# Performance work log

Hardware: AMD Instinct MI355X
Metric: run time of the kernel (lower is better)

## Reference

```python
import jax, jax.numpy as jnp
import numpy as np

B, T, D = 8, 4096, 768
H, HD, K = 12, 64, 32
TAU, THRESH = 12.5, 0.5
A_PARAM, B_PARAM, DT = 0.7, 0.8, 1.0  # nn.Parameters read via .item() -> scalar constants
N_FHN_STEPS = 2


def setup_inputs() -> dict:
    key = jax.random.key(0)
    k0, k1, k2, k3 = jax.random.split(key, 4)
    x = jax.random.normal(k0, (B, T, D), jnp.float32)
    spectral_basis = jax.random.normal(k1, (B, T, K), jnp.float32)
    w_qkv = jax.random.normal(k2, (3 * D, D), jnp.float32) * 0.02
    w_out = jax.random.normal(k3, (D, D), jnp.float32) * 0.02
    spectral_filter = jnp.ones((H, 32), jnp.float32) * 0.5
    return {"x": x, "spectral_basis": spectral_basis, "w_qkv": w_qkv,
            "w_out": w_out, "spectral_filter": spectral_filter}


def _fhn(stim):
    # Original expands stim [b,h,k] -> [b,h,k,head_dim] (constant along d), runs FHN,
    # then means over d. Values are identical along d, so amax over d == |stim| and the
    # mean is the identity; the math collapses exactly to per-element dynamics on [b,h,k].
    scale = jnp.maximum(jnp.abs(stim), 1e-6)          # == abs().amax(-1).clamp(1e-6)
    stim_normed = stim / scale
    gate = jax.nn.sigmoid((jnp.abs(stim) - THRESH) * 10.0)
    I = stim_normed * (0.1 + 0.9 * gate)
    alpha = DT / TAU
    denom = 1.0 + alpha * B_PARAM
    v = jnp.zeros_like(stim)
    w = jnp.zeros_like(stim)
    for _ in range(N_FHN_STEPS):  # fixed small n_steps, unrolled
        dv = v - (v * v * v) / 3.0 - w + I
        v_next = v + dv * DT
        w_next = (w + (v_next + A_PARAM) * alpha) / denom
        v = jnp.clip(v_next, -3.0, 3.0)
        w = jnp.clip(w_next, -3.0, 3.0)
    return v * scale


def reference(x, spectral_basis, w_qkv, w_out, spectral_filter):
    Bs, Ts, Ds = x.shape
    k = spectral_basis.shape[-1]
    qkv = x @ w_qkv.T                                   # [B,T,3D]
    qkv = qkv.reshape(Bs, Ts, 3, H, HD).transpose(2, 0, 3, 1, 4)  # three,b,h,t,d
    q, kk, v = qkv[0], qkv[1], qkv[2]
    q_spec = jnp.einsum('bhtd,btk->bhkd', q, spectral_basis)
    k_spec = jnp.einsum('bhtd,btk->bhkd', kk, spectral_basis)
    attn_spec = jnp.einsum('bhkd,bhkd->bhk', q_spec, k_spec) / (HD ** 0.5)
    filt = jax.nn.sigmoid(spectral_filter[:, :k])       # [H,k]
    attn_spec = attn_spec * filt[None, :, :]
    fhn_response = _fhn(attn_spec)                      # [B,H,k]
    v_spec = jnp.einsum('bhtd,btk->bhkd', v, spectral_basis)
    out_spec = fhn_response[..., None] * v_spec         # [B,H,k,d]
    out = jnp.einsum('bhkd,btk->bhtd', out_spec, spectral_basis)
    out = out.transpose(0, 2, 1, 3).reshape(Bs, Ts, Ds)  # b t (h d)
    return out @ w_out.T
```

## Files before the change

### kernel.cpp

```cpp
#include <hip/hip_runtime.h>

#define Bc 8
#define Tc 4096
#define Dc 768
#define Hc 12
#define HDc 64
#define Kc 32
#define TD3 2304
#define WQKV_F (TD3 * Dc)
#define WALL_F ((TD3 + Dc) * Dc)

typedef __attribute__((ext_vector_type(8))) short short8;
typedef __attribute__((ext_vector_type(4))) short short4v;
typedef __attribute__((ext_vector_type(4))) float float4v;

__device__ __forceinline__ float bf2f(unsigned short u) {
    unsigned v = ((unsigned)u) << 16;
    return __builtin_bit_cast(float, v);
}
__device__ __forceinline__ unsigned short f2bf(float f) {
    unsigned u = __builtin_bit_cast(unsigned, f);
    u += 0x7FFFu + ((u >> 16) & 1u);
    return (unsigned short)(u >> 16);
}

__device__ __forceinline__ void split8(const float* p, short8& hi, short8& lo) {
#pragma unroll
    for (int i = 0; i < 8; ++i) {
        unsigned short h = f2bf(p[i]);
        hi[i] = (short)h;
        lo[i] = (short)f2bf(p[i] - bf2f(h));
    }
}

__global__ __launch_bounds__(256) void k1_xspec(const float* __restrict__ x,
                                                const float* __restrict__ sb,
                                                float* __restrict__ pb) {
    __shared__ float xt[32 * 193];
    __shared__ float st[32 * 33];

    int tid  = threadIdx.x;
    int w    = tid >> 6;
    int lane = tid & 63;
    int col  = lane & 15;
    int quad = lane >> 4;

    int bid = blockIdx.x;
    int b  = bid >> 6;
    int dt = (bid >> 4) & 3;
    int tc = bid & 15;
    int d0 = dt * 192;
    size_t bT = (size_t)b * Tc + (size_t)tc * 256;

    float4v acc[2][3];
#pragma unroll
    for (int mi = 0; mi < 2; ++mi)
#pragma unroll
        for (int ni = 0; ni < 3; ++ni) acc[mi][ni] = (float4v){0.f, 0.f, 0.f, 0.f};

    for (int ks = 0; ks < 8; ++ks) {
        __syncthreads();
#pragma unroll
        for (int i = 0; i < 6; ++i) {
            int f4  = tid + i * 256;
            int row = f4 / 48, c4 = f4 % 48;
            float4v v = *(const float4v*)&x[(bT + ks * 32 + row) * Dc + d0 + c4 * 4];
#pragma unroll
            for (int q = 0; q < 4; ++q) xt[row * 193 + c4 * 4 + q] = v[q];
        }
        {
            int row = tid >> 3, c4 = tid & 7;
            float4v v = *(const float4v*)&sb[(bT + ks * 32 + row) * Kc + c4 * 4];
#pragma unroll
            for (int q = 0; q < 4; ++q) st[row * 33 + c4 * 4 + q] = v[q];
        }
        __syncthreads();

        short8 ah[2], al[2];
#pragma unroll
        for (int mi = 0; mi < 2; ++mi) {
            float av[8];
#pragma unroll
            for (int j = 0; j < 8; ++j)
                av[j] = st[(quad * 8 + j) * 33 + mi * 16 + col];
            split8(av, ah[mi], al[mi]);
        }
#pragma unroll
        for (int ni = 0; ni < 3; ++ni) {
            int nc = (w * 3 + ni) * 16 + col;
            float bv[8];
#pragma unroll
            for (int j = 0; j < 8; ++j)
                bv[j] = xt[(quad * 8 + j) * 193 + nc];
            short8 bh, bl;
            split8(bv, bh, bl);
#pragma unroll
            for (int mi = 0; mi < 2; ++mi) {
                acc[mi][ni] = __builtin_amdgcn_mfma_f32_16x16x32_bf16(ah[mi], bh, acc[mi][ni], 0, 0, 0);
                acc[mi][ni] = __builtin_amdgcn_mfma_f32_16x16x32_bf16(al[mi], bh, acc[mi][ni], 0, 0, 0);
                acc[mi][ni] = __builtin_amdgcn_mfma_f32_16x16x32_bf16(ah[mi], bl, acc[mi][ni], 0, 0, 0);
            }
        }
    }

    float* pbp = pb + (size_t)tc * (Bc * Kc * Dc);
#pragma unroll
    for (int mi = 0; mi < 2; ++mi)
#pragma unroll
        for (int ni = 0; ni < 3; ++ni)
#pragma unroll
            for (int r = 0; r < 4; ++r) {
                int kk = mi * 16 + quad * 4 + r;
                int dd = d0 + (w * 3 + ni) * 16 + col;
                pbp[((size_t)(b * Kc + kk)) * Dc + dd] = acc[mi][ni][r];
            }
}

__global__ __launch_bounds__(256) void k1r_reduce(const float* __restrict__ pb,
                                                  short* __restrict__ xs_hi,
                                                  short* __restrict__ xs_lo) {
    int i = (blockIdx.x * 256 + threadIdx.x) * 4;
    float4v s = (float4v){0.f, 0.f, 0.f, 0.f};
#pragma unroll
    for (int p = 0; p < 16; ++p) {
        float4v v = *(const float4v*)(pb + (size_t)p * (Bc * Kc * Dc) + i);
#pragma unroll
        for (int q = 0; q < 4; ++q) s[q] += v[q];
    }
    short4v h, l;
#pragma unroll
    for (int q = 0; q < 4; ++q) {
        unsigned short hb = f2bf(s[q]);
        h[q] = (short)hb;
        l[q] = (short)f2bf(s[q] - bf2f(hb));
    }
    *(short4v*)(xs_hi + i) = h;
    *(short4v*)(xs_lo + i) = l;
}

__global__ __launch_bounds__(256) void kconv(const float* __restrict__ wqkv,
                                             const float* __restrict__ wout,
                                             short* __restrict__ w_hi,
                                             short* __restrict__ w_lo) {
    int i = (blockIdx.x * 256 + threadIdx.x) * 4;
    const float* src = (i < WQKV_F) ? (wqkv + i) : (wout + (i - WQKV_F));
    float4v v = *(const float4v*)src;
    short4v h, l;
#pragma unroll
    for (int q = 0; q < 4; ++q) {
        unsigned short hb = f2bf(v[q]);
        h[q] = (short)hb;
        l[q] = (short)f2bf(v[q] - bf2f(hb));
    }
    *(short4v*)(w_hi + i) = h;
    *(short4v*)(w_lo + i) = l;
}

__global__ __launch_bounds__(256) void k2_qkv(const short* __restrict__ xs_hi,
                                              const short* __restrict__ xs_lo,
                                              const short* __restrict__ w_hi,
                                              const short* __restrict__ w_lo,
                                              float* __restrict__ c1) {
    int lane = threadIdx.x & 63;
    int w    = threadIdx.x >> 6;
    int m    = lane & 15, quad = lane >> 4;
    int mb = blockIdx.x & 7;
    int nb = blockIdx.x >> 3;
    int m0 = mb * 32;
    int n0 = nb * 64 + w * 16;

    const short* a0h = xs_hi + (size_t)(m0 + m) * Dc + quad * 8;
    const short* a0l = xs_lo + (size_t)(m0 + m) * Dc + quad * 8;
    const short* a1h = a0h + (size_t)16 * Dc;
    const short* a1l = a0l + (size_t)16 * Dc;
    const short* bhp = w_hi + (size_t)(n0 + m) * Dc + quad * 8;
    const short* blp = w_lo + (size_t)(n0 + m) * Dc + quad * 8;

    float4v acc0 = (float4v){0.f, 0.f, 0.f, 0.f};
    float4v acc1 = (float4v){0.f, 0.f, 0.f, 0.f};
#pragma unroll 4
    for (int s = 0; s < 24; ++s) {
        short8 bh = *(const short8*)(bhp + s * 32);
        short8 bl = *(const short8*)(blp + s * 32);
        short8 h0 = *(const short8*)(a0h + s * 32);
        short8 l0 = *(const short8*)(a0l + s * 32);
        short8 h1 = *(const short8*)(a1h + s * 32);
        short8 l1 = *(const short8*)(a1l + s * 32);
        acc0 = __builtin_amdgcn_mfma_f32_16x16x32_bf16(h0, bh, acc0, 0, 0, 0);
        acc0 = __builtin_amdgcn_mfma_f32_16x16x32_bf16(l0, bh, acc0, 0, 0, 0);
        acc0 = __builtin_amdgcn_mfma_f32_16x16x32_bf16(h0, bl, acc0, 0, 0, 0);
        acc1 = __builtin_amdgcn_mfma_f32_16x16x32_bf16(h1, bh, acc1, 0, 0, 0);
        acc1 = __builtin_amdgcn_mfma_f32_16x16x32_bf16(l1, bh, acc1, 0, 0, 0);
        acc1 = __builtin_amdgcn_mfma_f32_16x16x32_bf16(h1, bl, acc1, 0, 0, 0);
    }
    float* cp0 = c1 + (size_t)(m0 + quad * 4) * TD3 + n0 + m;
    float* cp1 = cp0 + (size_t)16 * TD3;
#pragma unroll
    for (int r = 0; r < 4; ++r) {
        cp0[(size_t)r * TD3] = acc0[r];
        cp1[(size_t)r * TD3] = acc1[r];
    }
}

__global__ __launch_bounds__(256) void k3_fhn(const float* __restrict__ c1,
                                              const float* __restrict__ sfilt,
                                              float* __restrict__ fhn) {
    int idx = blockIdx.x * 256 + threadIdx.x;
    if (idx >= Bc * Hc * Kc) return;
    int kk = idx & 31;
    int bh = idx >> 5;
    int h  = bh % Hc;
    int r  = (bh / Hc) * Kc + kk;

    const float* qp = c1 + (size_t)r * TD3 + h * HDc;
    const float* kp = qp + Dc;
    float s = 0.f;
#pragma unroll
    for (int dd = 0; dd < HDc; ++dd) s = fmaf(qp[dd], kp[dd], s);
    s *= 0.125f;

    float filt = 1.f / (1.f + __expf(-sfilt[h * 32 + kk]));
    s *= filt;

    float as    = fabsf(s);
    float scale = fmaxf(as, 1e-6f);
    float sn    = s / scale;
    float gate  = 1.f / (1.f + __expf(-(as - 0.5f) * 10.f));
    float I     = sn * (0.1f + 0.9f * gate);
    const float alpha = 0.08f;
    const float denom = 1.064f;
    float v = 0.f, w = 0.f;
#pragma unroll
    for (int it = 0; it < 2; ++it) {
        float dv = v - (v * v * v) / 3.f - w + I;
        float vn = v + dv;
        float wn = (w + (vn + 0.7f) * alpha) / denom;
        v = fminf(fmaxf(vn, -3.f), 3.f);
        w = fminf(fmaxf(wn, -3.f), 3.f);
    }
    fhn[idx] = v * scale;
}

__global__ __launch_bounds__(256) void k4_proj(const float* __restrict__ c1,
                                               const float* __restrict__ fhn,
                                               const short* __restrict__ wo_hi,
                                               const short* __restrict__ wo_lo,
                                               float* __restrict__ proj) {
    int wave = blockIdx.x * 4 + (threadIdx.x >> 6);
    int lane = threadIdx.x & 63;
    int mb = wave & 15;
    int nt = wave >> 4;
    int m0 = mb * 16, n0 = nt * 16;
    int m = lane & 15, quad = lane >> 4;

    const short* bhp = wo_hi + (size_t)(n0 + m) * Dc + quad * 8;
    const short* blp = wo_lo + (size_t)(n0 + m) * Dc + quad * 8;

    int r = m0 + m;
    int b = r >> 5, kk = r & 31;
    const float* apx = c1 + (size_t)r * TD3 + 2 * Dc + quad * 8;
    const float* fp  = fhn + (size_t)b * Hc * Kc + kk;

    float4v acc = (float4v){0.f, 0.f, 0.f, 0.f};
#pragma unroll 4
    for (int s = 0; s < 24; ++s) {
        int h = (s * 32 + quad * 8) >> 6;
        float f = fp[h * Kc];
        float av[8];
#pragma unroll
        for (int i = 0; i < 8; ++i) av[i] = apx[s * 32 + i] * f;
        short8 ah, al;
        split8(av, ah, al);
        short8 bh = *(const short8*)(bhp + s * 32);
        short8 bl = *(const short8*)(blp + s * 32);
        acc = __builtin_amdgcn_mfma_f32_16x16x32_bf16(ah, bh, acc, 0, 0, 0);
        acc = __builtin_amdgcn_mfma_f32_16x16x32_bf16(al, bh, acc, 0, 0, 0);
        acc = __builtin_amdgcn_mfma_f32_16x16x32_bf16(ah, bl, acc, 0, 0, 0);
    }
    float* cp = proj + (size_t)(m0 + quad * 4) * Dc + n0 + m;
#pragma unroll
    for (int rr = 0; rr < 4; ++rr) cp[(size_t)rr * Dc] = acc[rr];
}

__global__ __launch_bounds__(256) void k5_out(const float* __restrict__ proj,
                                              const float* __restrict__ sb,
                                              float* __restrict__ out) {
    __shared__ float pt[32 * 193];

    int tid  = threadIdx.x;
    int w    = tid >> 6;
    int lane = tid & 63;
    int col  = lane & 15;
    int quad = lane >> 4;

    int bid = blockIdx.x;
    int b  = bid >> 8;
    int tt = (bid >> 2) & 63;
    int et = bid & 3;
    int t0 = tt * 64 + w * 16;
    int e0 = et * 192;

#pragma unroll
    for (int i = 0; i < 6; ++i) {
        int f4  = tid + i * 256;
        int row = f4 / 48, c4 = f4 % 48;
        float4v v = *(const float4v*)&proj[(size_t)b * Kc * Dc + (size_t)row * Dc + e0 + c4 * 4];
#pragma unroll
        for (int q = 0; q < 4; ++q) pt[row * 193 + c4 * 4 + q] = v[q];
    }

    const float* apx = sb + ((size_t)b * Tc + t0 + col) * Kc + quad * 8;
    short8 ah, al;
    split8(apx, ah, al);

    __syncthreads();

    float4v acc[12];
#pragma unroll
    for (int ni = 0; ni < 12; ++ni) acc[ni] = (float4v){0.f, 0.f, 0.f, 0.f};

#pragma unroll
    for (int ni = 0; ni < 12; ++ni) {
        float bv[8];
#pragma unroll
        for (int j = 0; j < 8; ++j)
            bv[j] = pt[(quad * 8 + j) * 193 + ni * 16 + col];
        short8 bh, bl;
        split8(bv, bh, bl);
        acc[ni] = __builtin_amdgcn_mfma_f32_16x16x32_bf16(ah, bh, acc[ni], 0, 0, 0);
        acc[ni] = __builtin_amdgcn_mfma_f32_16x16x32_bf16(al, bh, acc[ni], 0, 0, 0);
        acc[ni] = __builtin_amdgcn_mfma_f32_16x16x32_bf16(ah, bl, acc[ni], 0, 0, 0);
    }

    float* op = out + ((size_t)b * Tc + t0 + quad * 4) * Dc + e0 + col;
#pragma unroll
    for (int ni = 0; ni < 12; ++ni)
#pragma unroll
        for (int r = 0; r < 4; ++r)
            op[(size_t)r * Dc + ni * 16] = acc[ni][r];
}

extern "C" void kernel_launch(void* const* d_in, const int* in_sizes, int n_in,
                              void* d_out, int out_size, void* d_ws, size_t ws_size,
                              hipStream_t stream) {
    const float* x     = (const float*)d_in[0];
    const float* sb    = (const float*)d_in[1];
    const float* wqkv  = (const float*)d_in[2];
    const float* wout  = (const float*)d_in[3];
    const float* sfilt = (const float*)d_in[4];
    float* out = (float*)d_out;

    float* pb   = (float*)d_ws;
    short* w_hi = (short*)d_ws;
    short* w_lo = w_hi + (size_t)WALL_F;
    float* base = pb + (size_t)16 * Bc * Kc * Dc;
    short* xs_hi = (short*)base;
    short* xs_lo = xs_hi + (size_t)Bc * Kc * Dc;
    float* c1   = base + (size_t)Bc * Kc * Dc;
    float* fhn  = c1 + (size_t)Bc * Kc * TD3;
    float* proj = fhn + (size_t)Bc * Hc * Kc;

    const short* wo_hi = w_hi + (size_t)WQKV_F;
    const short* wo_lo = w_lo + (size_t)WQKV_F;

    hipLaunchKernelGGL(k1_xspec,   dim3(512),  dim3(256), 0, stream, x, sb, pb);
    hipLaunchKernelGGL(k1r_reduce, dim3(192),  dim3(256), 0, stream, pb, xs_hi, xs_lo);
    hipLaunchKernelGGL(kconv,      dim3(2304), dim3(256), 0, stream, wqkv, wout, w_hi, w_lo);
    hipLaunchKernelGGL(k2_qkv,     dim3(288),  dim3(256), 0, stream, xs_hi, xs_lo, w_hi, w_lo, c1);
    hipLaunchKernelGGL(k3_fhn,     dim3(12),   dim3(256), 0, stream, c1, sfilt, fhn);
    hipLaunchKernelGGL(k4_proj,    dim3(192),  dim3(256), 0, stream, c1, fhn, wo_hi, wo_lo, proj);
    hipLaunchKernelGGL(k5_out,     dim3(2048), dim3(256), 0, stream, proj, sb, out);
}
```

Baseline: 264.7 us.

## Pre-split spectral basis into bf16 hi/lo plus transpose; drop LDS staging in k1/k5

The weight conversion kernel now also splits the spectral basis into bf16 hi/lo pairs, in both the original and a transposed layout. k1 reads the transposed basis directly and loads x straight from global memory, with no shared-memory staging or barriers. The FHN kernel folds the response scaling into V and writes pre-split bf16 operands, and k4 writes its projection pre-split and transposed so k5 can load MFMA fragments directly without LDS. The aim is to remove repeated fp32-to-bf16 splitting and LDS traffic. The cost is extra workspace, an uncoalesced scattered transpose write in kconv, and strided global loads of x in k1.

```diff
diff --git a/kernel.cpp b/kernel.cpp
--- a/kernel.cpp
+++ b/kernel.cpp
@@ -9,6 +9,8 @@
 #define TD3 2304
 #define WQKV_F (TD3 * Dc)
 #define WALL_F ((TD3 + Dc) * Dc)
+#define SB_F (Bc * Tc * Kc)
+#define XS_F (Bc * Kc * Dc)
 
 typedef __attribute__((ext_vector_type(8))) short short8;
 typedef __attribute__((ext_vector_type(4))) short short4v;
@@ -32,13 +34,52 @@
         lo[i] = (short)f2bf(p[i] - bf2f(h));
     }
 }
+__device__ __forceinline__ void split4(const float4v v, short4v& h, short4v& l) {
+#pragma unroll
+    for (int q = 0; q < 4; ++q) {
+        unsigned short hb = f2bf(v[q]);
+        h[q] = (short)hb;
+        l[q] = (short)f2bf(v[q] - bf2f(hb));
+    }
+}
+
+__global__ __launch_bounds__(256) void kconv(const float* __restrict__ wqkv,
+                                             const float* __restrict__ wout,
+                                             const float* __restrict__ sb,
+                                             short* __restrict__ w_hi, short* __restrict__ w_lo,
+                                             short* __restrict__ sb_hi, short* __restrict__ sb_lo,
+                                             short* __restrict__ sbT_hi, short* __restrict__ sbT_lo) {
+    int i = (blockIdx.x * 256 + threadIdx.x) * 4;
+    if (i < WALL_F) {
+        const float* src = (i < WQKV_F) ? (wqkv + i) : (wout + (i - WQKV_F));
+        float4v v = *(const float4v*)src;
+        short4v h, l;
+        split4(v, h, l);
+        *(short4v*)(w_hi + i) = h;
+        *(short4v*)(w_lo + i) = l;
+    } else {
+        int j = i - WALL_F;
+        float4v v = *(const float4v*)(sb + j);
+        short4v h, l;
+        split4(v, h, l);
+        *(short4v*)(sb_hi + j) = h;
+        *(short4v*)(sb_lo + j) = l;
+        int b   = j >> 17;
+        int rem = j & (Tc * Kc - 1);
+        int t = rem >> 5, k = rem & 31;
+        size_t tb = (size_t)b * Kc * Tc;
+#pragma unroll
+        for (int q = 0; q < 4; ++q) {
+            sbT_hi[tb + (size_t)(k + q) * Tc + t] = h[q];
+            sbT_lo[tb + (size_t)(k + q) * Tc + t] = l[q];
+        }
+    }
+}
 
 __global__ __launch_bounds__(256) void k1_xspec(const float* __restrict__ x,
-                                                const float* __restrict__ sb,
+                                                const short* __restrict__ sbT_hi,
+                                                const short* __restrict__ sbT_lo,
                                                 float* __restrict__ pb) {
-    __shared__ float xt[32 * 193];
-    __shared__ float st[32 * 33];
-
     int tid  = threadIdx.x;
     int w    = tid >> 6;
     int lane = tid & 63;
@@ -58,40 +99,23 @@
 #pragma unroll
         for (int ni = 0; ni < 3; ++ni) acc[mi][ni] = (float4v){0.f, 0.f, 0.f, 0.f};
 
+#pragma unroll 2
     for (int ks = 0; ks < 8; ++ks) {
-        __syncthreads();
-#pragma unroll
-        for (int i = 0; i < 6; ++i) {
-            int f4  = tid + i * 256;
-            int row = f4 / 48, c4 = f4 % 48;
-            float4v v = *(const float4v*)&x[(bT + ks * 32 + row) * Dc + d0 + c4 * 4];
-#pragma unroll
-            for (int q = 0; q < 4; ++q) xt[row * 193 + c4 * 4 + q] = v[q];
+        int t8 = tc * 256 + ks * 32 + quad * 8;
+        short8 ah[2], al[2];
+#pragma unroll
+        for (int mi = 0; mi < 2; ++mi) {
+            size_t ai = ((size_t)b * Kc + mi * 16 + col) * Tc + t8;
+            ah[mi] = *(const short8*)(sbT_hi + ai);
+            al[mi] = *(const short8*)(sbT_lo + ai);
         }
-        {
-            int row = tid >> 3, c4 = tid & 7;
-            float4v v = *(const float4v*)&sb[(bT + ks * 32 + row) * Kc + c4 * 4];
-#pragma unroll
-            for (int q = 0; q < 4; ++q) st[row * 33 + c4 * 4 + q] = v[q];
-        }
-        __syncthreads();
-
-        short8 ah[2], al[2];
-#pragma unroll
-        for (int mi = 0; mi < 2; ++mi) {
-            float av[8];
+#pragma unroll
+        for (int ni = 0; ni < 3; ++ni) {
+            int nc = d0 + (w * 3 + ni) * 16 + col;
+            float bv[8];
 #pragma unroll
             for (int j = 0; j < 8; ++j)
-                av[j] = st[(quad * 8 + j) * 33 + mi * 16 + col];
-            split8(av, ah[mi], al[mi]);
-        }
-#pragma unroll
-        for (int ni = 0; ni < 3; ++ni) {
-            int nc = (w * 3 + ni) * 16 + col;
-            float bv[8];
-#pragma unroll
-            for (int j = 0; j < 8; ++j)
-                bv[j] = xt[(quad * 8 + j) * 193 + nc];
+                bv[j] = x[(bT + ks * 32 + quad * 8 + j) * Dc + nc];
             short8 bh, bl;
             split8(bv, bh, bl);
 #pragma unroll
@@ -103,7 +127,7 @@
         }
     }
 
-    float* pbp = pb + (size_t)tc * (Bc * Kc * Dc);
+    float* pbp = pb + (size_t)tc * XS_F;
 #pragma unroll
     for (int mi = 0; mi < 2; ++mi)
 #pragma unroll
@@ -123,37 +147,14 @@
     float4v s = (float4v){0.f, 0.f, 0.f, 0.f};
 #pragma unroll
     for (int p = 0; p < 16; ++p) {
-        float4v v = *(const float4v*)(pb + (size_t)p * (Bc * Kc * Dc) + i);
+        float4v v = *(const float4v*)(pb + (size_t)p * XS_F + i);
 #pragma unroll
         for (int q = 0; q < 4; ++q) s[q] += v[q];
     }
     short4v h, l;
-#pragma unroll
-    for (int q = 0; q < 4; ++q) {
-        unsigned short hb = f2bf(s[q]);
-        h[q] = (short)hb;
-        l[q] = (short)f2bf(s[q] - bf2f(hb));
-    }
+    split4(s, h, l);
     *(short4v*)(xs_hi + i) = h;
     *(short4v*)(xs_lo + i) = l;
-}
-
-__global__ __launch_bounds__(256) void kconv(const float* __restrict__ wqkv,
-                                             const float* __restrict__ wout,
-                                             short* __restrict__ w_hi,
-                                             short* __restrict__ w_lo) {
-    int i = (blockIdx.x * 256 + threadIdx.x) * 4;
-    const float* src = (i < WQKV_F) ? (wqkv + i) : (wout + (i - WQKV_F));
-    float4v v = *(const float4v*)src;
-    short4v h, l;
-#pragma unroll
-    for (int q = 0; q < 4; ++q) {
-        unsigned short hb = f2bf(v[q]);
-        h[q] = (short)hb;
-        l[q] = (short)f2bf(v[q] - bf2f(hb));
-    }
-    *(short4v*)(w_hi + i) = h;
-    *(short4v*)(w_lo + i) = l;
 }
 
 __global__ __launch_bounds__(256) void k2_qkv(const short* __restrict__ xs_hi,
@@ -202,11 +203,11 @@
     }
 }
 
-__global__ __launch_bounds__(256) void k3_fhn(const float* __restrict__ c1,
-                                              const float* __restrict__ sfilt,
-                                              float* __restrict__ fhn) {
-    int idx = blockIdx.x * 256 + threadIdx.x;
-    if (idx >= Bc * Hc * Kc) return;
+__global__ __launch_bounds__(64) void k3_fhn(const float* __restrict__ c1,
+                                             const float* __restrict__ sfilt,
+                                             short* __restrict__ av_hi,
+                                             short* __restrict__ av_lo) {
+    int idx = blockIdx.x * 64 + threadIdx.x;
     int kk = idx & 31;
     int bh = idx >> 5;
     int h  = bh % Hc;
@@ -238,14 +239,29 @@
         v = fminf(fmaxf(vn, -3.f), 3.f);
         w = fminf(fmaxf(wn, -3.f), 3.f);
     }
-    fhn[idx] = v * scale;
-}
-
-__global__ __launch_bounds__(256) void k4_proj(const float* __restrict__ c1,
-                                               const float* __restrict__ fhn,
+    float fv = v * scale;
+
+    const float* vp = c1 + (size_t)r * TD3 + 2 * Dc + h * HDc;
+    short* ohp = av_hi + (size_t)r * Dc + h * HDc;
+    short* olp = av_lo + (size_t)r * Dc + h * HDc;
+#pragma unroll
+    for (int i = 0; i < 16; ++i) {
+        float4v vv = *(const float4v*)(vp + i * 4);
+#pragma unroll
+        for (int q = 0; q < 4; ++q) vv[q] *= fv;
+        short4v hv, lv;
+        split4(vv, hv, lv);
+        *(short4v*)(ohp + i * 4) = hv;
+        *(short4v*)(olp + i * 4) = lv;
+    }
+}
+
+__global__ __launch_bounds__(256) void k4_proj(const short* __restrict__ av_hi,
+                                               const short* __restrict__ av_lo,
                                                const short* __restrict__ wo_hi,
                                                const short* __restrict__ wo_lo,
-                                               float* __restrict__ proj) {
+                                               short* __restrict__ pT_hi,
+                                               short* __restrict__ pT_lo) {
     int wave = blockIdx.x * 4 + (threadIdx.x >> 6);
     int lane = threadIdx.x & 63;
     int mb = wave & 15;
@@ -253,40 +269,34 @@
     int m0 = mb * 16, n0 = nt * 16;
     int m = lane & 15, quad = lane >> 4;
 
+    const short* ahp = av_hi + (size_t)(m0 + m) * Dc + quad * 8;
+    const short* alp = av_lo + (size_t)(m0 + m) * Dc + quad * 8;
     const short* bhp = wo_hi + (size_t)(n0 + m) * Dc + quad * 8;
     const short* blp = wo_lo + (size_t)(n0 + m) * Dc + quad * 8;
-
-    int r = m0 + m;
-    int b = r >> 5, kk = r & 31;
-    const float* apx = c1 + (size_t)r * TD3 + 2 * Dc + quad * 8;
-    const float* fp  = fhn + (size_t)b * Hc * Kc + kk;
 
     float4v acc = (float4v){0.f, 0.f, 0.f, 0.f};
 #pragma unroll 4
     for (int s = 0; s < 24; ++s) {
-        int h = (s * 32 + quad * 8) >> 6;
-        float f = fp[h * Kc];
-        float av[8];
-#pragma unroll
-        for (int i = 0; i < 8; ++i) av[i] = apx[s * 32 + i] * f;
-        short8 ah, al;
-        split8(av, ah, al);
+        short8 ah = *(const short8*)(ahp + s * 32);
+        short8 al = *(const short8*)(alp + s * 32);
         short8 bh = *(const short8*)(bhp + s * 32);
         short8 bl = *(const short8*)(blp + s * 32);
         acc = __builtin_amdgcn_mfma_f32_16x16x32_bf16(ah, bh, acc, 0, 0, 0);
         acc = __builtin_amdgcn_mfma_f32_16x16x32_bf16(al, bh, acc, 0, 0, 0);
         acc = __builtin_amdgcn_mfma_f32_16x16x32_bf16(ah, bl, acc, 0, 0, 0);
     }
-    float* cp = proj + (size_t)(m0 + quad * 4) * Dc + n0 + m;
-#pragma unroll
-    for (int rr = 0; rr < 4; ++rr) cp[(size_t)rr * Dc] = acc[rr];
-}
-
-__global__ __launch_bounds__(256) void k5_out(const float* __restrict__ proj,
-                                              const float* __restrict__ sb,
+    short4v hv, lv;
+    split4(acc, hv, lv);
+    size_t o = (size_t)(n0 + m) * (Bc * Kc) + m0 + quad * 4;
+    *(short4v*)(pT_hi + o) = hv;
+    *(short4v*)(pT_lo + o) = lv;
+}
+
+__global__ __launch_bounds__(256) void k5_out(const short* __restrict__ pT_hi,
+                                              const short* __restrict__ pT_lo,
+                                              const short* __restrict__ sb_hi,
+                                              const short* __restrict__ sb_lo,
                                               float* __restrict__ out) {
-    __shared__ float pt[32 * 193];
-
     int tid  = threadIdx.x;
     int w    = tid >> 6;
     int lane = tid & 63;
@@ -300,20 +310,9 @@
     int t0 = tt * 64 + w * 16;
     int e0 = et * 192;
 
-#pragma unroll
-    for (int i = 0; i < 6; ++i) {
-        int f4  = tid + i * 256;
-        int row = f4 / 48, c4 = f4 % 48;
-        float4v v = *(const float4v*)&proj[(size_t)b * Kc * Dc + (size_t)row * Dc + e0 + c4 * 4];
-#pragma unroll
-        for (int q = 0; q < 4; ++q) pt[row * 193 + c4 * 4 + q] = v[q];
-    }
-
-    const float* apx = sb + ((size_t)b * Tc + t0 + col) * Kc + quad * 8;
-    short8 ah, al;
-    split8(apx, ah, al);
-
-    __syncthreads();
+    size_t ao = ((size_t)b * Tc + t0 + col) * Kc + quad * 8;
+    short8 ah = *(const short8*)(sb_hi + ao);
+    short8 al = *(const short8*)(sb_lo + ao);
 
     float4v acc[12];
 #pragma unroll
@@ -321,12 +320,9 @@
 
 #pragma unroll
     for (int ni = 0; ni < 12; ++ni) {
-        float bv[8];
-#pragma unroll
-        for (int j = 0; j < 8; ++j)
-            bv[j] = pt[(quad * 8 + j) * 193 + ni * 16 + col];
-        short8 bh, bl;
-        split8(bv, bh, bl);
+        size_t bo = (size_t)(e0 + ni * 16 + col) * (Bc * Kc) + b * 32 + quad * 8;
+        short8 bh = *(const short8*)(pT_hi + bo);
+        short8 bl = *(const short8*)(pT_lo + bo);
         acc[ni] = __builtin_amdgcn_mfma_f32_16x16x32_bf16(ah, bh, acc[ni], 0, 0, 0);
         acc[ni] = __builtin_amdgcn_mfma_f32_16x16x32_bf16(al, bh, acc[ni], 0, 0, 0);
         acc[ni] = __builtin_amdgcn_mfma_f32_16x16x32_bf16(ah, bl, acc[ni], 0, 0, 0);
@@ -350,24 +346,30 @@
     const float* sfilt = (const float*)d_in[4];
     float* out = (float*)d_out;
 
-    float* pb   = (float*)d_ws;
-    short* w_hi = (short*)d_ws;
-    short* w_lo = w_hi + (size_t)WALL_F;
-    float* base = pb + (size_t)16 * Bc * Kc * Dc;
-    short* xs_hi = (short*)base;
-    short* xs_lo = xs_hi + (size_t)Bc * Kc * Dc;
-    float* c1   = base + (size_t)Bc * Kc * Dc;
-    float* fhn  = c1 + (size_t)Bc * Kc * TD3;
-    float* proj = fhn + (size_t)Bc * Hc * Kc;
+    float* pb    = (float*)d_ws;
+    short* w_hi  = (short*)(pb + (size_t)16 * XS_F);
+    short* w_lo  = w_hi + (size_t)WALL_F;
+    short* xs_hi = w_lo + (size_t)WALL_F;
+    short* xs_lo = xs_hi + (size_t)XS_F;
+    float* c1    = (float*)(xs_lo + (size_t)XS_F);
+    short* av_hi = (short*)(c1 + (size_t)Bc * Kc * TD3);
+    short* av_lo = av_hi + (size_t)XS_F;
+    short* pT_hi = av_lo + (size_t)XS_F;
+    short* pT_lo = pT_hi + (size_t)XS_F;
+    short* sb_hi = pT_lo + (size_t)XS_F;
+    short* sb_lo = sb_hi + (size_t)SB_F;
+    short* sbT_hi = sb_lo + (size_t)SB_F;
+    short* sbT_lo = sbT_hi + (size_t)SB_F;
 
     const short* wo_hi = w_hi + (size_t)WQKV_F;
     const short* wo_lo = w_lo + (size_t)WQKV_F;
 
-    hipLaunchKernelGGL(k1_xspec,   dim3(512),  dim3(256), 0, stream, x, sb, pb);
+    hipLaunchKernelGGL(kconv,      dim3(3328), dim3(256), 0, stream, wqkv, wout, sb,
+                       w_hi, w_lo, sb_hi, sb_lo, sbT_hi, sbT_lo);
+    hipLaunchKernelGGL(k1_xspec,   dim3(512),  dim3(256), 0, stream, x, sbT_hi, sbT_lo, pb);
     hipLaunchKernelGGL(k1r_reduce, dim3(192),  dim3(256), 0, stream, pb, xs_hi, xs_lo);
-    hipLaunchKernelGGL(kconv,      dim3(2304), dim3(256), 0, stream, wqkv, wout, w_hi, w_lo);
     hipLaunchKernelGGL(k2_qkv,     dim3(288),  dim3(256), 0, stream, xs_hi, xs_lo, w_hi, w_lo, c1);
-    hipLaunchKernelGGL(k3_fhn,     dim3(12),   dim3(256), 0, stream, c1, sfilt, fhn);
-    hipLaunchKernelGGL(k4_proj,    dim3(192),  dim3(256), 0, stream, c1, fhn, wo_hi, wo_lo, proj);
-    hipLaunchKernelGGL(k5_out,     dim3(2048), dim3(256), 0, stream, proj, sb, out);
-}
+    hipLaunchKernelGGL(k3_fhn,     dim3(48),   dim3(64),  0, stream, c1, sfilt, av_hi, av_lo);
+    hipLaunchKernelGGL(k4_proj,    dim3(192),  dim3(256), 0, stream, av_hi, av_lo, wo_hi, wo_lo, pT_hi, pT_lo);
+    hipLaunchKernelGGL(k5_out,     dim3(2048), dim3(256), 0, stream, pT_hi, pT_lo, sb_hi, sb_lo, out);
+}
```

Result: slower. 284.4 us (+7.4%).
